# Performance work log

Measured on AMD Instinct MI355X. Metric: run time of the kernel, lower is better.

## Reference

```python
import jax, jax.numpy as jnp
import numpy as np

N_NODES = 10000
N_EDGES = 160000
D_IN = 512
D_OUT = 512

def setup_inputs() -> dict:
    key = jax.random.key(0)
    k1, k2, k3, k4, k5 = jax.random.split(key, 5)
    feature = jax.random.normal(k1, (N_NODES, D_IN), dtype=jnp.float32)
    src = jax.random.randint(k2, (N_EDGES,), 0, N_NODES, dtype=jnp.int64)
    dst = jax.random.randint(k3, (N_EDGES,), 0, N_NODES, dtype=jnp.int64)
    # Linear(2*in_feats -> out_feats): stored as [2*D_IN, D_OUT] for x @ W + b
    W = jax.random.normal(k4, (2 * D_IN, D_OUT), dtype=jnp.float32) * (1.0 / np.sqrt(2 * D_IN))
    b = jax.random.normal(k5, (D_OUT,), dtype=jnp.float32) * 0.01
    return {"feature": feature, "src": src, "dst": dst, "W": W, "b": b}

def reference(feature, src, dst, W, b):
    n = feature.shape[0]
    # update_all(copy_src('h'), sum -> 'neigh'): scatter-add src features onto dst
    neigh = jax.ops.segment_sum(feature[src], dst, num_segments=n)  # [N, D_IN]
    # in_degrees(): count of incoming edges per node
    degs = jax.ops.segment_sum(jnp.ones_like(dst, dtype=feature.dtype), dst, num_segments=n)
    # clamp to 1 to avoid 0/0 for isolated nodes (sum is 0 there, so result is 0 either way)
    hk_neigh = neigh / jnp.maximum(degs, 1.0)[:, None]
    hk = jnp.concatenate([feature, hk_neigh], axis=-1) @ W + b  # [N, D_OUT]
    return jax.nn.relu(hk)
```

## Files before the change

kernel.cpp:

```cpp
#include <hip/hip_runtime.h>
#include <hip/hip_bf16.h>


#define N_NODES 10000
#define N_EDGES 160000
#define D_IN    512
#define D_OUT   512
#define K_DIM   1024

typedef float  f32x4  __attribute__((ext_vector_type(4)));
typedef __bf16 bf16x8 __attribute__((ext_vector_type(8)));
typedef unsigned short us8 __attribute__((ext_vector_type(8)));
typedef unsigned short us4 __attribute__((ext_vector_type(4)));

__device__ __forceinline__ unsigned short f2b(float f) {
    unsigned int u = __float_as_uint(f);
    unsigned int r = u + 0x7FFFu + ((u >> 16) & 1u);
    return (unsigned short)(r >> 16);
}
__device__ __forceinline__ float b2f(unsigned short h) {
    return __uint_as_float(((unsigned int)h) << 16);
}
__device__ __forceinline__ void gl_lds16(const void* g, void* l) {
    auto gp = (const __attribute__((address_space(1))) unsigned int*)(uintptr_t)g;
    auto lp = (__attribute__((address_space(3))) unsigned int*)(uintptr_t)l;
    __builtin_amdgcn_global_load_lds(gp, lp, 16, 0, 0);
}

__global__ __launch_bounds__(256) void wtrans_kernel(const float* __restrict__ W,
                                                     unsigned short* __restrict__ WbT,
                                                     int* __restrict__ cnt) {
    const int kt = blockIdx.x;
    const int nt = blockIdx.y;
    const int t  = threadIdx.x;

    const int bid = nt * 32 + kt;
    const int zi  = bid * 20 + t;
    if (t < 20 && zi < N_NODES) cnt[zi] = 0;

    __shared__ float tile[32][33];
    const int c  = t & 31;
    const int r0 = t >> 5;
#pragma unroll
    for (int p = 0; p < 4; ++p) {
        int r = r0 + p * 8;
        tile[r][c] = W[(size_t)(kt * 32 + r) * D_OUT + nt * 32 + c];
    }
    __syncthreads();
#pragma unroll
    for (int p = 0; p < 4; ++p) {
        int r = r0 + p * 8;
        WbT[(size_t)(nt * 32 + r) * K_DIM + kt * 32 + c] = f2b(tile[c][r]);
    }
}

__global__ __launch_bounds__(256) void convert_hist_kernel(const float* __restrict__ feat,
                                                           const int* __restrict__ dst,
                                                           unsigned short* __restrict__ Xb,
                                                           int* __restrict__ cnt) {
    const int gid = blockIdx.x * 256 + threadIdx.x;
    const int row = gid >> 6;
    const int l   = gid & 63;
    const float4* s = (const float4*)(feat + (size_t)row * D_IN + l * 8);
    float4 v0 = s[0], v1 = s[1];
    us8 o;
    o[0] = f2b(v0.x); o[1] = f2b(v0.y); o[2] = f2b(v0.z); o[3] = f2b(v0.w);
    o[4] = f2b(v1.x); o[5] = f2b(v1.y); o[6] = f2b(v1.z); o[7] = f2b(v1.w);
    *(us8*)(Xb + (size_t)row * K_DIM + l * 8) = o;
    if (gid < N_EDGES) atomicAdd(&cnt[dst[gid]], 1);
}

__global__ __launch_bounds__(256) void scan_kernel(const int* __restrict__ cnt,
                                                   int* __restrict__ rowstart,
                                                   int* __restrict__ cursor) {
    __shared__ int sums[256];
    const int t = threadIdx.x;
    const int base = t * 40;
    const int4* c4 = (const int4*)(cnt + base);
    int s = 0;
    if (base < N_NODES) {
#pragma unroll
        for (int i = 0; i < 10; ++i) {
            int4 v = c4[i];
            s += v.x + v.y + v.z + v.w;
        }
    }
    sums[t] = s;
    __syncthreads();
    for (int off = 1; off < 256; off <<= 1) {
        int v = (t >= off) ? sums[t - off] : 0;
        __syncthreads();
        sums[t] += v;
        __syncthreads();
    }
    int run = (t == 0) ? 0 : sums[t - 1];
    if (base < N_NODES) {
        int4* r4 = (int4*)(rowstart + base);
        int4* u4 = (int4*)(cursor + base);
#pragma unroll
        for (int i = 0; i < 10; ++i) {
            int4 v = c4[i];
            int4 o;
            o.x = run;  o.y = run + v.x;  o.z = run + v.x + v.y;
            o.w = run + v.x + v.y + v.z;
            run += v.x + v.y + v.z + v.w;
            r4[i] = o;
            u4[i] = o;
        }
    }
    if (t == 255) rowstart[N_NODES] = sums[255];
}

__global__ __launch_bounds__(256) void bucket_kernel(const int* __restrict__ src,
                                                     const int* __restrict__ dst,
                                                     int* __restrict__ cursor,
                                                     int* __restrict__ eidx) {
    int e = blockIdx.x * 256 + threadIdx.x;
    int d = dst[e];
    int slot = atomicAdd(&cursor[d], 1);
    eidx[slot] = src[e];
}

__global__ __launch_bounds__(256) void gather_kernel(unsigned short* Xb,
                                                     const int* __restrict__ eidx,
                                                     const int* __restrict__ rowstart) {
    const int wv   = threadIdx.x >> 6;
    const int l    = threadIdx.x & 63;
    const int node = blockIdx.x * 2 + (wv >> 1);
    const int half = wv & 1;
    const int col  = half * 256 + l * 4;
    const int beg  = rowstart[node];
    const int end  = rowstart[node + 1];
    float a0 = 0.f, a1 = 0.f, a2 = 0.f, a3 = 0.f;
    int j = beg;
    for (; j + 4 <= end; j += 4) {
        int s0 = eidx[j], s1 = eidx[j + 1], s2 = eidx[j + 2], s3 = eidx[j + 3];
        us4 v0 = *(const us4*)(Xb + (size_t)s0 * K_DIM + col);
        us4 v1 = *(const us4*)(Xb + (size_t)s1 * K_DIM + col);
        us4 v2 = *(const us4*)(Xb + (size_t)s2 * K_DIM + col);
        us4 v3 = *(const us4*)(Xb + (size_t)s3 * K_DIM + col);
        a0 += (b2f(v0[0]) + b2f(v1[0])) + (b2f(v2[0]) + b2f(v3[0]));
        a1 += (b2f(v0[1]) + b2f(v1[1])) + (b2f(v2[1]) + b2f(v3[1]));
        a2 += (b2f(v0[2]) + b2f(v1[2])) + (b2f(v2[2]) + b2f(v3[2]));
        a3 += (b2f(v0[3]) + b2f(v1[3])) + (b2f(v2[3]) + b2f(v3[3]));
    }
    for (; j < end; ++j) {
        int s0 = eidx[j];
        us4 v0 = *(const us4*)(Xb + (size_t)s0 * K_DIM + col);
        a0 += b2f(v0[0]); a1 += b2f(v0[1]); a2 += b2f(v0[2]); a3 += b2f(v0[3]);
    }
    float sc = 1.0f / fmaxf((float)(end - beg), 1.0f);
    us4 o;
    o[0] = f2b(a0 * sc); o[1] = f2b(a1 * sc); o[2] = f2b(a2 * sc); o[3] = f2b(a3 * sc);
    *(us4*)(Xb + (size_t)node * K_DIM + D_IN + col) = o;
}

__global__ __launch_bounds__(256, 2) void gemm_kernel(const unsigned short* __restrict__ Xb,
                                                      const unsigned short* __restrict__ WbT,
                                                      const float* __restrict__ bias,
                                                      float* __restrict__ out) {
    __shared__ __align__(16) unsigned short As[2][8192];
    __shared__ __align__(16) unsigned short Bs[2][8192];

    const int p    = blockIdx.x;
    const int xcd  = p & 7;
    const int rank = p >> 3;
    const int g    = xcd + 8 * (rank >> 2);
    const int c    = rank & 3;
    if (g >= 79) return;
    const int brow = g * 128;
    const int bcol = c * 128;

    const int tid = threadIdx.x;
    const int l   = tid & 63;
    const int w   = tid >> 6;
    const int wr  = w >> 1, wc = w & 1;

    const int sub  = l >> 3;
    const int scol = ((l & 7) * 16) ^ (sub * 16);
    const char* pa[4];
    const char* pb[4];
#pragma unroll
    for (int q = 0; q < 4; ++q) {
        int ra = brow + q * 32 + w * 8 + sub;
        ra = ra < N_NODES ? ra : N_NODES - 1;
        pa[q] = (const char*)Xb + (size_t)ra * 2048 + scol;
        pb[q] = (const char*)WbT + (size_t)(bcol + q * 32 + w * 8 + sub) * 2048 + scol;
    }

#define STAGE(buf, koff) do {                                          \
        gl_lds16(pa[0] + (koff), &As[buf][(0 * 32 + w * 8) * 64]);     \
        gl_lds16(pa[1] + (koff), &As[buf][(1 * 32 + w * 8) * 64]);     \
        gl_lds16(pa[2] + (koff), &As[buf][(2 * 32 + w * 8) * 64]);     \
        gl_lds16(pa[3] + (koff), &As[buf][(3 * 32 + w * 8) * 64]);     \
        gl_lds16(pb[0] + (koff), &Bs[buf][(0 * 32 + w * 8) * 64]);     \
        gl_lds16(pb[1] + (koff), &Bs[buf][(1 * 32 + w * 8) * 64]);     \
        gl_lds16(pb[2] + (koff), &Bs[buf][(2 * 32 + w * 8) * 64]);     \
        gl_lds16(pb[3] + (koff), &Bs[buf][(3 * 32 + w * 8) * 64]);     \
    } while (0)

    const int fr = l & 15;
    const int gq = l >> 4;
    const int sw = (fr & 7) * 16;
    const int h0 = ((gq * 16)      ^ sw) >> 1;
    const int h1 = ((64 + gq * 16) ^ sw) >> 1;

    f32x4 acc[4][4] = {};

    STAGE(0, 0);
    __syncthreads();
    int cur = 0;
#pragma unroll 2
    for (int t = 0; t < 16; ++t) {
        if (t < 15) STAGE(cur ^ 1, (t + 1) * 128);
        bf16x8 a[4][2], b[4][2];
#pragma unroll
        for (int m = 0; m < 4; ++m) {
            int r = (wr * 64 + m * 16 + fr) * 64;
            a[m][0] = *(const bf16x8*)&As[cur][r + h0];
            a[m][1] = *(const bf16x8*)&As[cur][r + h1];
        }
#pragma unroll
        for (int n = 0; n < 4; ++n) {
            int r = (wc * 64 + n * 16 + fr) * 64;
            b[n][0] = *(const bf16x8*)&Bs[cur][r + h0];
            b[n][1] = *(const bf16x8*)&Bs[cur][r + h1];
        }
#pragma unroll
        for (int kh = 0; kh < 2; ++kh)
#pragma unroll
            for (int m = 0; m < 4; ++m)
#pragma unroll
                for (int n = 0; n < 4; ++n)
                    acc[m][n] = __builtin_amdgcn_mfma_f32_16x16x32_bf16(a[m][kh], b[n][kh], acc[m][n], 0, 0, 0);
        __syncthreads();
        cur ^= 1;
    }
#undef STAGE

#pragma unroll
    for (int n = 0; n < 4; ++n) {
        int col = bcol + wc * 64 + n * 16 + fr;
        float bv = bias[col];
#pragma unroll
        for (int m = 0; m < 4; ++m) {
            int row0 = brow + wr * 64 + m * 16 + gq * 4;
#pragma unroll
            for (int j = 0; j < 4; ++j) {
                int row = row0 + j;
                if (row < N_NODES)
                    out[(size_t)row * D_OUT + col] = fmaxf(acc[m][n][j] + bv, 0.0f);
            }
        }
    }
}

extern "C" void kernel_launch(void* const* d_in, const int* in_sizes, int n_in,
                              void* d_out, int out_size, void* d_ws, size_t ws_size,
                              hipStream_t stream) {
    const float* feat = (const float*)d_in[0];
    const int*   src  = (const int*)d_in[1];
    const int*   dst  = (const int*)d_in[2];
    const float* W    = (const float*)d_in[3];
    const float* bias = (const float*)d_in[4];
    float*       out  = (float*)d_out;

    char* ws = (char*)d_ws;
    unsigned short* Xb  = (unsigned short*)(ws);
    int*   cnt          = (int*)(ws + 20480000);
    int*   rowstart     = (int*)(ws + 20520000);
    int*   cursor       = (int*)(ws + 20560016);
    int*   eidx         = (int*)(ws + 20600032);
    unsigned short* WbT = (unsigned short*)(ws + 21240032);

    wtrans_kernel<<<dim3(32, 16), 256, 0, stream>>>(W, WbT, cnt);
    convert_hist_kernel<<<2500, 256, 0, stream>>>(feat, dst, Xb, cnt);
    scan_kernel<<<1, 256, 0, stream>>>(cnt, rowstart, cursor);
    bucket_kernel<<<N_EDGES / 256, 256, 0, stream>>>(src, dst, cursor, eidx);
    gather_kernel<<<5000, 256, 0, stream>>>(Xb, eidx, rowstart);
    gemm_kernel<<<320, 256, 0, stream>>>(Xb, WbT, bias, out);
}
```

Measured before the change: 89.24 us.

## Fuse prefix scan into histogram kernel via last-block-done counter; unroll gather by 8

The single-block scan kernel is folded into the convert/histogram kernel. Every block bumps a global done counter, and the last block to arrive performs the degree prefix scan, which removes one kernel launch and its dependency gap. The scan reads the counts through atomics to see the other blocks' results, which makes that tail serial work slower. The gather loop also gains an 8-way unrolled path so more neighbour loads are in flight at once, at the cost of more registers.

```diff
diff --git a/kernel.cpp b/kernel.cpp
--- a/kernel.cpp
+++ b/kernel.cpp
@@ -29,7 +29,8 @@
 
 __global__ __launch_bounds__(256) void wtrans_kernel(const float* __restrict__ W,
                                                      unsigned short* __restrict__ WbT,
-                                                     int* __restrict__ cnt) {
+                                                     int* __restrict__ cnt,
+                                                     int* __restrict__ done) {
     const int kt = blockIdx.x;
     const int nt = blockIdx.y;
     const int t  = threadIdx.x;
@@ -37,6 +38,7 @@
     const int bid = nt * 32 + kt;
     const int zi  = bid * 20 + t;
     if (t < 20 && zi < N_NODES) cnt[zi] = 0;
+    if (t == 20 && bid == 0) *done = 0;
 
     __shared__ float tile[32][33];
     const int c  = t & 31;
@@ -54,58 +56,66 @@
     }
 }
 
-__global__ __launch_bounds__(256) void convert_hist_kernel(const float* __restrict__ feat,
-                                                           const int* __restrict__ dst,
-                                                           unsigned short* __restrict__ Xb,
-                                                           int* __restrict__ cnt) {
-    const int gid = blockIdx.x * 256 + threadIdx.x;
-    const int row = gid >> 6;
-    const int l   = gid & 63;
-    const float4* s = (const float4*)(feat + (size_t)row * D_IN + l * 8);
-    float4 v0 = s[0], v1 = s[1];
-    us8 o;
-    o[0] = f2b(v0.x); o[1] = f2b(v0.y); o[2] = f2b(v0.z); o[3] = f2b(v0.w);
-    o[4] = f2b(v1.x); o[5] = f2b(v1.y); o[6] = f2b(v1.z); o[7] = f2b(v1.w);
-    *(us8*)(Xb + (size_t)row * K_DIM + l * 8) = o;
+__global__ __launch_bounds__(256) void convert_hist_scan_kernel(const float* __restrict__ feat,
+                                                                const int* __restrict__ dst,
+                                                                unsigned short* __restrict__ Xb,
+                                                                int* __restrict__ cnt,
+                                                                int* __restrict__ rowstart,
+                                                                int* __restrict__ cursor,
+                                                                int* __restrict__ done) {
+    const int b = blockIdx.x;
+    const int t = threadIdx.x;
+    const int gid = b * 256 + t;
+
+    {
+        const int row = gid >> 6;
+        const int l   = gid & 63;
+        const float4* s = (const float4*)(feat + (size_t)row * D_IN + l * 8);
+        float4 v0 = s[0], v1 = s[1];
+        us8 o;
+        o[0] = f2b(v0.x); o[1] = f2b(v0.y); o[2] = f2b(v0.z); o[3] = f2b(v0.w);
+        o[4] = f2b(v1.x); o[5] = f2b(v1.y); o[6] = f2b(v1.z); o[7] = f2b(v1.w);
+        *(us8*)(Xb + (size_t)row * K_DIM + l * 8) = o;
+    }
     if (gid < N_EDGES) atomicAdd(&cnt[dst[gid]], 1);
-}
-
-__global__ __launch_bounds__(256) void scan_kernel(const int* __restrict__ cnt,
-                                                   int* __restrict__ rowstart,
-                                                   int* __restrict__ cursor) {
+
     __shared__ int sums[256];
-    const int t = threadIdx.x;
+    __shared__ int isLast;
+    __threadfence();
+    __syncthreads();
+    if (t == 0) {
+        int old = atomicAdd(done, 1);
+        isLast = (old == 2499) ? 1 : 0;
+    }
+    __syncthreads();
+    if (!isLast) return;
+
     const int base = t * 40;
-    const int4* c4 = (const int4*)(cnt + base);
+    int v[40];
     int s = 0;
-    if (base < N_NODES) {
-#pragma unroll
-        for (int i = 0; i < 10; ++i) {
-            int4 v = c4[i];
-            s += v.x + v.y + v.z + v.w;
-        }
+#pragma unroll
+    for (int i = 0; i < 40; ++i) {
+        int idx = base + i;
+        int x = (idx < N_NODES) ? atomicAdd(&cnt[idx], 0) : 0;
+        v[i] = x;
+        s += x;
     }
     sums[t] = s;
     __syncthreads();
     for (int off = 1; off < 256; off <<= 1) {
-        int v = (t >= off) ? sums[t - off] : 0;
+        int x = (t >= off) ? sums[t - off] : 0;
         __syncthreads();
-        sums[t] += v;
+        sums[t] += x;
         __syncthreads();
     }
     int run = (t == 0) ? 0 : sums[t - 1];
-    if (base < N_NODES) {
-        int4* r4 = (int4*)(rowstart + base);
-        int4* u4 = (int4*)(cursor + base);
-#pragma unroll
-        for (int i = 0; i < 10; ++i) {
-            int4 v = c4[i];
-            int4 o;
-            o.x = run;  o.y = run + v.x;  o.z = run + v.x + v.y;
-            o.w = run + v.x + v.y + v.z;
-            run += v.x + v.y + v.z + v.w;
-            r4[i] = o;
-            u4[i] = o;
+#pragma unroll
+    for (int i = 0; i < 40; ++i) {
+        int idx = base + i;
+        if (idx < N_NODES) {
+            rowstart[idx] = run;
+            cursor[idx]   = run;
+            run += v[i];
         }
     }
     if (t == 255) rowstart[N_NODES] = sums[255];
@@ -133,20 +143,36 @@
     const int end  = rowstart[node + 1];
     float a0 = 0.f, a1 = 0.f, a2 = 0.f, a3 = 0.f;
     int j = beg;
+    for (; j + 8 <= end; j += 8) {
+        us4 v0 = *(const us4*)(Xb + (size_t)eidx[j]     * K_DIM + col);
+        us4 v1 = *(const us4*)(Xb + (size_t)eidx[j + 1] * K_DIM + col);
+        us4 v2 = *(const us4*)(Xb + (size_t)eidx[j + 2] * K_DIM + col);
+        us4 v3 = *(const us4*)(Xb + (size_t)eidx[j + 3] * K_DIM + col);
+        us4 v4 = *(const us4*)(Xb + (size_t)eidx[j + 4] * K_DIM + col);
+        us4 v5 = *(const us4*)(Xb + (size_t)eidx[j + 5] * K_DIM + col);
+        us4 v6 = *(const us4*)(Xb + (size_t)eidx[j + 6] * K_DIM + col);
+        us4 v7 = *(const us4*)(Xb + (size_t)eidx[j + 7] * K_DIM + col);
+        a0 += ((b2f(v0[0]) + b2f(v1[0])) + (b2f(v2[0]) + b2f(v3[0])))
+            + ((b2f(v4[0]) + b2f(v5[0])) + (b2f(v6[0]) + b2f(v7[0])));
+        a1 += ((b2f(v0[1]) + b2f(v1[1])) + (b2f(v2[1]) + b2f(v3[1])))
+            + ((b2f(v4[1]) + b2f(v5[1])) + (b2f(v6[1]) + b2f(v7[1])));
+        a2 += ((b2f(v0[2]) + b2f(v1[2])) + (b2f(v2[2]) + b2f(v3[2])))
+            + ((b2f(v4[2]) + b2f(v5[2])) + (b2f(v6[2]) + b2f(v7[2])));
+        a3 += ((b2f(v0[3]) + b2f(v1[3])) + (b2f(v2[3]) + b2f(v3[3])))
+            + ((b2f(v4[3]) + b2f(v5[3])) + (b2f(v6[3]) + b2f(v7[3])));
+    }
     for (; j + 4 <= end; j += 4) {
-        int s0 = eidx[j], s1 = eidx[j + 1], s2 = eidx[j + 2], s3 = eidx[j + 3];
-        us4 v0 = *(const us4*)(Xb + (size_t)s0 * K_DIM + col);
-        us4 v1 = *(const us4*)(Xb + (size_t)s1 * K_DIM + col);
-        us4 v2 = *(const us4*)(Xb + (size_t)s2 * K_DIM + col);
-        us4 v3 = *(const us4*)(Xb + (size_t)s3 * K_DIM + col);
+        us4 v0 = *(const us4*)(Xb + (size_t)eidx[j]     * K_DIM + col);
+        us4 v1 = *(const us4*)(Xb + (size_t)eidx[j + 1] * K_DIM + col);
+        us4 v2 = *(const us4*)(Xb + (size_t)eidx[j + 2] * K_DIM + col);
+        us4 v3 = *(const us4*)(Xb + (size_t)eidx[j + 3] * K_DIM + col);
         a0 += (b2f(v0[0]) + b2f(v1[0])) + (b2f(v2[0]) + b2f(v3[0]));
         a1 += (b2f(v0[1]) + b2f(v1[1])) + (b2f(v2[1]) + b2f(v3[1]));
         a2 += (b2f(v0[2]) + b2f(v1[2])) + (b2f(v2[2]) + b2f(v3[2]));
         a3 += (b2f(v0[3]) + b2f(v1[3])) + (b2f(v2[3]) + b2f(v3[3]));
     }
     for (; j < end; ++j) {
-        int s0 = eidx[j];
-        us4 v0 = *(const us4*)(Xb + (size_t)s0 * K_DIM + col);
+        us4 v0 = *(const us4*)(Xb + (size_t)eidx[j] * K_DIM + col);
         a0 += b2f(v0[0]); a1 += b2f(v0[1]); a2 += b2f(v0[2]); a3 += b2f(v0[3]);
     }
     float sc = 1.0f / fmaxf((float)(end - beg), 1.0f);
@@ -272,10 +298,11 @@
     int*   cursor       = (int*)(ws + 20560016);
     int*   eidx         = (int*)(ws + 20600032);
     unsigned short* WbT = (unsigned short*)(ws + 21240032);
-
-    wtrans_kernel<<<dim3(32, 16), 256, 0, stream>>>(W, WbT, cnt);
-    convert_hist_kernel<<<2500, 256, 0, stream>>>(feat, dst, Xb, cnt);
-    scan_kernel<<<1, 256, 0, stream>>>(cnt, rowstart, cursor);
+    int*   done         = (int*)(ws + 22288608);
+
+    wtrans_kernel<<<dim3(32, 16), 256, 0, stream>>>(W, WbT, cnt, done);
+    convert_hist_scan_kernel<<<2500, 256, 0, stream>>>(feat, dst, Xb, cnt,
+                                                       rowstart, cursor, done);
     bucket_kernel<<<N_EDGES / 256, 256, 0, stream>>>(src, dst, cursor, eidx);
     gather_kernel<<<5000, 256, 0, stream>>>(Xb, eidx, rowstart);
     gemm_kernel<<<320, 256, 0, stream>>>(Xb, WbT, bias, out);
```

New measurement: 304.2 us. 241% more time.

## Shrink GEMM N-tile to 64, double grid, and unroll gather by 8

Applied to the files above, without the earlier changes.

The GEMM tile changes from 128x128 to 128x64, and the grid doubles to 640 blocks with an 8-way column mapping. The B staging buffer is halved and launch bounds rise to 3 blocks per CU, giving more parallelism on the 256-CU device at the cost of reloading A tiles more often. The gather kernel now splits the two column halves across separate block ranges, each wave handling one node. Its inner loop is unrolled to 8 edges to keep more loads in flight.

```diff
diff --git a/kernel.cpp b/kernel.cpp
--- a/kernel.cpp
+++ b/kernel.cpp
@@ -126,27 +126,34 @@
                                                      const int* __restrict__ rowstart) {
     const int wv   = threadIdx.x >> 6;
     const int l    = threadIdx.x & 63;
-    const int node = blockIdx.x * 2 + (wv >> 1);
-    const int half = wv & 1;
+    const int half = (blockIdx.x >= 2500) ? 1 : 0;
+    const int b    = blockIdx.x - half * 2500;
+    const int node = b * 4 + wv;
     const int col  = half * 256 + l * 4;
     const int beg  = rowstart[node];
     const int end  = rowstart[node + 1];
     float a0 = 0.f, a1 = 0.f, a2 = 0.f, a3 = 0.f;
     int j = beg;
-    for (; j + 4 <= end; j += 4) {
-        int s0 = eidx[j], s1 = eidx[j + 1], s2 = eidx[j + 2], s3 = eidx[j + 3];
-        us4 v0 = *(const us4*)(Xb + (size_t)s0 * K_DIM + col);
-        us4 v1 = *(const us4*)(Xb + (size_t)s1 * K_DIM + col);
-        us4 v2 = *(const us4*)(Xb + (size_t)s2 * K_DIM + col);
-        us4 v3 = *(const us4*)(Xb + (size_t)s3 * K_DIM + col);
-        a0 += (b2f(v0[0]) + b2f(v1[0])) + (b2f(v2[0]) + b2f(v3[0]));
-        a1 += (b2f(v0[1]) + b2f(v1[1])) + (b2f(v2[1]) + b2f(v3[1]));
-        a2 += (b2f(v0[2]) + b2f(v1[2])) + (b2f(v2[2]) + b2f(v3[2]));
-        a3 += (b2f(v0[3]) + b2f(v1[3])) + (b2f(v2[3]) + b2f(v3[3]));
+    for (; j + 8 <= end; j += 8) {
+        us4 v0 = *(const us4*)(Xb + (size_t)eidx[j]     * K_DIM + col);
+        us4 v1 = *(const us4*)(Xb + (size_t)eidx[j + 1] * K_DIM + col);
+        us4 v2 = *(const us4*)(Xb + (size_t)eidx[j + 2] * K_DIM + col);
+        us4 v3 = *(const us4*)(Xb + (size_t)eidx[j + 3] * K_DIM + col);
+        us4 v4 = *(const us4*)(Xb + (size_t)eidx[j + 4] * K_DIM + col);
+        us4 v5 = *(const us4*)(Xb + (size_t)eidx[j + 5] * K_DIM + col);
+        us4 v6 = *(const us4*)(Xb + (size_t)eidx[j + 6] * K_DIM + col);
+        us4 v7 = *(const us4*)(Xb + (size_t)eidx[j + 7] * K_DIM + col);
+        a0 += ((b2f(v0[0]) + b2f(v1[0])) + (b2f(v2[0]) + b2f(v3[0])))
+            + ((b2f(v4[0]) + b2f(v5[0])) + (b2f(v6[0]) + b2f(v7[0])));
+        a1 += ((b2f(v0[1]) + b2f(v1[1])) + (b2f(v2[1]) + b2f(v3[1])))
+            + ((b2f(v4[1]) + b2f(v5[1])) + (b2f(v6[1]) + b2f(v7[1])));
+        a2 += ((b2f(v0[2]) + b2f(v1[2])) + (b2f(v2[2]) + b2f(v3[2])))
+            + ((b2f(v4[2]) + b2f(v5[2])) + (b2f(v6[2]) + b2f(v7[2])));
+        a3 += ((b2f(v0[3]) + b2f(v1[3])) + (b2f(v2[3]) + b2f(v3[3])))
+            + ((b2f(v4[3]) + b2f(v5[3])) + (b2f(v6[3]) + b2f(v7[3])));
     }
     for (; j < end; ++j) {
-        int s0 = eidx[j];
-        us4 v0 = *(const us4*)(Xb + (size_t)s0 * K_DIM + col);
+        us4 v0 = *(const us4*)(Xb + (size_t)eidx[j] * K_DIM + col);
         a0 += b2f(v0[0]); a1 += b2f(v0[1]); a2 += b2f(v0[2]); a3 += b2f(v0[3]);
     }
     float sc = 1.0f / fmaxf((float)(end - beg), 1.0f);
@@ -155,21 +162,21 @@
     *(us4*)(Xb + (size_t)node * K_DIM + D_IN + col) = o;
 }
 
-__global__ __launch_bounds__(256, 2) void gemm_kernel(const unsigned short* __restrict__ Xb,
+__global__ __launch_bounds__(256, 3) void gemm_kernel(const unsigned short* __restrict__ Xb,
                                                       const unsigned short* __restrict__ WbT,
                                                       const float* __restrict__ bias,
                                                       float* __restrict__ out) {
     __shared__ __align__(16) unsigned short As[2][8192];
-    __shared__ __align__(16) unsigned short Bs[2][8192];
+    __shared__ __align__(16) unsigned short Bs[2][4096];
 
     const int p    = blockIdx.x;
     const int xcd  = p & 7;
     const int rank = p >> 3;
-    const int g    = xcd + 8 * (rank >> 2);
-    const int c    = rank & 3;
+    const int g    = xcd + 8 * (rank >> 3);
+    const int c    = rank & 7;
     if (g >= 79) return;
     const int brow = g * 128;
-    const int bcol = c * 128;
+    const int bcol = c * 64;
 
     const int tid = threadIdx.x;
     const int l   = tid & 63;
@@ -179,14 +186,16 @@
     const int sub  = l >> 3;
     const int scol = ((l & 7) * 16) ^ (sub * 16);
     const char* pa[4];
-    const char* pb[4];
+    const char* pb[2];
 #pragma unroll
     for (int q = 0; q < 4; ++q) {
         int ra = brow + q * 32 + w * 8 + sub;
         ra = ra < N_NODES ? ra : N_NODES - 1;
         pa[q] = (const char*)Xb + (size_t)ra * 2048 + scol;
+    }
+#pragma unroll
+    for (int q = 0; q < 2; ++q)
         pb[q] = (const char*)WbT + (size_t)(bcol + q * 32 + w * 8 + sub) * 2048 + scol;
-    }
 
 #define STAGE(buf, koff) do {                                          \
         gl_lds16(pa[0] + (koff), &As[buf][(0 * 32 + w * 8) * 64]);     \
@@ -195,8 +204,6 @@
         gl_lds16(pa[3] + (koff), &As[buf][(3 * 32 + w * 8) * 64]);     \
         gl_lds16(pb[0] + (koff), &Bs[buf][(0 * 32 + w * 8) * 64]);     \
         gl_lds16(pb[1] + (koff), &Bs[buf][(1 * 32 + w * 8) * 64]);     \
-        gl_lds16(pb[2] + (koff), &Bs[buf][(2 * 32 + w * 8) * 64]);     \
-        gl_lds16(pb[3] + (koff), &Bs[buf][(3 * 32 + w * 8) * 64]);     \
     } while (0)
 
     const int fr = l & 15;
@@ -205,7 +212,7 @@
     const int h0 = ((gq * 16)      ^ sw) >> 1;
     const int h1 = ((64 + gq * 16) ^ sw) >> 1;
 
-    f32x4 acc[4][4] = {};
+    f32x4 acc[4][2] = {};
 
     STAGE(0, 0);
     __syncthreads();
@@ -213,7 +220,7 @@
 #pragma unroll 2
     for (int t = 0; t < 16; ++t) {
         if (t < 15) STAGE(cur ^ 1, (t + 1) * 128);
-        bf16x8 a[4][2], b[4][2];
+        bf16x8 a[4][2], b[2][2];
 #pragma unroll
         for (int m = 0; m < 4; ++m) {
             int r = (wr * 64 + m * 16 + fr) * 64;
@@ -221,8 +228,8 @@
             a[m][1] = *(const bf16x8*)&As[cur][r + h1];
         }
 #pragma unroll
-        for (int n = 0; n < 4; ++n) {
-            int r = (wc * 64 + n * 16 + fr) * 64;
+        for (int n = 0; n < 2; ++n) {
+            int r = (wc * 32 + n * 16 + fr) * 64;
             b[n][0] = *(const bf16x8*)&Bs[cur][r + h0];
             b[n][1] = *(const bf16x8*)&Bs[cur][r + h1];
         }
@@ -231,7 +238,7 @@
 #pragma unroll
             for (int m = 0; m < 4; ++m)
 #pragma unroll
-                for (int n = 0; n < 4; ++n)
+                for (int n = 0; n < 2; ++n)
                     acc[m][n] = __builtin_amdgcn_mfma_f32_16x16x32_bf16(a[m][kh], b[n][kh], acc[m][n], 0, 0, 0);
         __syncthreads();
         cur ^= 1;
@@ -239,8 +246,8 @@
 #undef STAGE
 
 #pragma unroll
-    for (int n = 0; n < 4; ++n) {
-        int col = bcol + wc * 64 + n * 16 + fr;
+    for (int n = 0; n < 2; ++n) {
+        int col = bcol + wc * 32 + n * 16 + fr;
         float bv = bias[col];
 #pragma unroll
         for (int m = 0; m < 4; ++m) {
@@ -278,5 +285,5 @@
     scan_kernel<<<1, 256, 0, stream>>>(cnt, rowstart, cursor);
     bucket_kernel<<<N_EDGES / 256, 256, 0, stream>>>(src, dst, cursor, eidx);
     gather_kernel<<<5000, 256, 0, stream>>>(Xb, eidx, rowstart);
-    gemm_kernel<<<320, 256, 0, stream>>>(Xb, WbT, bias, out);
-}
+    gemm_kernel<<<640, 256, 0, stream>>>(Xb, WbT, bias, out);
+}
```

New measurement: 86.07 us. -3.6%, faster.
